# Performance work log

Measured on AMD Instinct MI355X. Metric: run time of the kernel, lower is better.

Reference implementation:

```python
import jax, jax.numpy as jnp
from jax import lax
import numpy as np

B, T, I, H, O = 256, 1024, 64, 25, 64

def setup_inputs() -> dict:
    key = jax.random.key(0)
    ks = jax.random.split(key, 7)
    s_ih = 1.0 / np.sqrt(H)  # PyTorch LSTM init scale (uniform +-1/sqrt(H))
    return {
        "x": jax.random.normal(ks[0], (B, T, I), dtype=jnp.float32),
        "W_ih": jax.random.uniform(ks[1], (4 * H, I), minval=-s_ih, maxval=s_ih, dtype=jnp.float32),
        "W_hh": jax.random.uniform(ks[2], (4 * H, H), minval=-s_ih, maxval=s_ih, dtype=jnp.float32),
        "b_ih": jax.random.uniform(ks[3], (4 * H,), minval=-s_ih, maxval=s_ih, dtype=jnp.float32),
        "b_hh": jax.random.uniform(ks[4], (4 * H,), minval=-s_ih, maxval=s_ih, dtype=jnp.float32),
        "W_fc": jax.random.uniform(ks[5], (O, H), minval=-s_ih, maxval=s_ih, dtype=jnp.float32),
        "b_fc": jax.random.uniform(ks[6], (O,), minval=-s_ih, maxval=s_ih, dtype=jnp.float32),
    }

def reference(x, W_ih, W_hh, b_ih, b_hh, W_fc, b_fc):
    # x: [B, T, I]; PyTorch LSTM gate order: i, f, g, o
    Bh = x.shape[0]
    Hh = W_hh.shape[1]
    # Precompute the input contribution to all gates for all timesteps (one big GEMM).
    gates_x = jnp.einsum('bti,gi->btg', x, W_ih) + b_ih + b_hh  # [B, T, 4H]

    def step(carry, gx):
        h, c = carry
        g = gx + h @ W_hh.T                     # [B, 4H]
        i, f, gg, o = jnp.split(g, 4, axis=-1)
        i = jax.nn.sigmoid(i)
        f = jax.nn.sigmoid(f)
        gg = jnp.tanh(gg)
        o = jax.nn.sigmoid(o)
        c = f * c + i * gg
        h = o * jnp.tanh(c)
        return (h, c), h

    h0 = jnp.zeros((Bh, Hh), dtype=x.dtype)
    c0 = jnp.zeros((Bh, Hh), dtype=x.dtype)
    _, hs = lax.scan(step, (h0, c0), jnp.swapaxes(gates_x, 0, 1))  # hs: [T, B, H]
    hs = jnp.swapaxes(hs, 0, 1)                                   # [B, T, H]
    return hs @ W_fc.T + b_fc                                     # [B, T, O]
```

## Files before the change

kernel.cpp:

```cpp
#include <hip/hip_runtime.h>
#include <hip/hip_fp16.h>


#define Bn 256
#define Tn 1024
#define In 64
#define Hn 25
#define Gn 100
#define On 64
#define BT (Bn * Tn)
#define ROW 100

#define SCL_S -1.44269504089f
#define SCL_T -2.88539008178f

typedef __attribute__((ext_vector_type(8))) short short8;
typedef __attribute__((ext_vector_type(4))) float f32x4;

__device__ __forceinline__ float frcp(float x) { return __builtin_amdgcn_rcpf(x); }
__device__ __forceinline__ float ex2(float x) {
    float r;
    asm("v_exp_f32 %0, %1\n\ts_nop 1" : "=v"(r) : "v"(x));
    return r;
}
__device__ __forceinline__ float bcast(float v, int lane) {
    return __int_as_float(__builtin_amdgcn_readlane(__float_as_int(v), lane));
}
__device__ __forceinline__ float xswap(float x) {
    float a = x, b = x;
    asm("s_nop 0\n\tv_permlane32_swap_b32 %0, %1\n\ts_nop 0"
        : "+v"(a), "+v"(b));
    return b;
}
__device__ __forceinline__ short f2bf(float f) {
    unsigned u = __float_as_uint(f);
    unsigned r = (u + 0x7FFFu + ((u >> 16) & 1u)) >> 16;
    return (short)r;
}

__device__ __forceinline__ void colmap(int n, int& g, float& scl) {
    if (n < 50) {
        const int r = n >> 1;
        g = ((n & 1) ? 2 : 0) * Hn + r;
        scl = (n & 1) ? SCL_T : SCL_S;
    } else {
        const int m = n - 50, r = m >> 1;
        g = ((m & 1) ? 3 : 1) * Hn + r;
        scl = SCL_S;
    }
}

__global__ __launch_bounds__(256)
void prep_w(const float* __restrict__ W_ih, const float* __restrict__ b_ih,
            const float* __restrict__ b_hh, short* __restrict__ wprep,
            float* __restrict__ bprep) {
    const int tid = threadIdx.x;
    for (int i = tid; i < 112 * 64; i += 256) {
        const int n = i >> 6, k = i & 63;
        float v = 0.f;
        if (n < Gn) {
            int g; float scl;
            colmap(n, g, scl);
            v = W_ih[(size_t)g * In + k] * scl;
        }
        wprep[i] = f2bf(v);
    }
    if (tid < 112) {
        float v = 0.f;
        if (tid < Gn) {
            int g; float scl;
            colmap(tid, g, scl);
            v = (b_ih[g] + b_hh[g]) * scl;
        }
        bprep[tid] = v;
    }
}

template <typename ST, bool PREP>
__global__ __launch_bounds__(256, 4)
void gates_mfma(const float* __restrict__ x, const float* __restrict__ W_ih,
                const float* __restrict__ b_ih, const float* __restrict__ b_hh,
                const short* __restrict__ wprep, const float* __restrict__ bprep,
                ST* __restrict__ gws) {
    __shared__ short lA[64 * 72];
    __shared__ short lB[112 * 72];
    __shared__ float lbias[112];

    const int tid = threadIdx.x;
    const size_t row0 = (size_t)blockIdx.x * 64;

    for (int i = tid; i < 64 * 64; i += 256) {
        const int r = i >> 6, k = i & 63;
        lA[r * 72 + k] = f2bf(x[(row0 + r) * In + k]);
    }
    if (PREP) {
        for (int i = tid; i < 112 * 32; i += 256) {
            const int j = 2 * i, n = j >> 6, k = j & 63;
            *(int*)&lB[n * 72 + k] = ((const int*)wprep)[i];
        }
        if (tid < 112) lbias[tid] = bprep[tid];
    } else {
        for (int i = tid; i < 112 * 64; i += 256) {
            const int n = i >> 6, k = i & 63;
            float v = 0.f;
            if (n < Gn) {
                int g; float scl;
                colmap(n, g, scl);
                v = W_ih[(size_t)g * In + k] * scl;
            }
            lB[n * 72 + k] = f2bf(v);
        }
        if (tid < 112) {
            float v = 0.f;
            if (tid < Gn) {
                int g; float scl;
                colmap(tid, g, scl);
                v = (b_ih[g] + b_hh[g]) * scl;
            }
            lbias[tid] = v;
        }
    }
    __syncthreads();

    const int wave = tid >> 6;
    const int lane = tid & 63;
    const int quad = lane >> 4;
    const int l16  = lane & 15;
    const int arow = wave * 16 + l16;

    const short8 a0 = *(const short8*)&lA[arow * 72 + 0  + quad * 8];
    const short8 a1 = *(const short8*)&lA[arow * 72 + 32 + quad * 8];

#pragma unroll
    for (int nt = 0; nt < 7; ++nt) {
        const int col = nt * 16 + l16;
        const short8 b0 = *(const short8*)&lB[col * 72 + 0  + quad * 8];
        const short8 b1 = *(const short8*)&lB[col * 72 + 32 + quad * 8];
        const float bias = lbias[col];
        f32x4 acc = {bias, bias, bias, bias};
        acc = __builtin_amdgcn_mfma_f32_16x16x32_bf16(a0, b0, acc, 0, 0, 0);
        acc = __builtin_amdgcn_mfma_f32_16x16x32_bf16(a1, b1, acc, 0, 0, 0);
        if (col < Gn) {
#pragma unroll
            for (int i = 0; i < 4; ++i) {
                const size_t grow = row0 + wave * 16 + quad * 4 + i;
                gws[grow * ROW + col] = (ST)acc[i];
            }
        }
    }
}

template <typename ST> struct GLD;
template <> struct GLD<float> {
    static __device__ __forceinline__ float2 ld(const float* base, int u) {
        return ((const float2*)base)[u];
    }
};
template <> struct GLD<__half> {
    static __device__ __forceinline__ float2 ld(const __half* base, int u) {
        const __half2 h = ((const __half2*)base)[u];
        return make_float2(__low2float(h), __high2float(h));
    }
};

template <typename ST>
__global__ __launch_bounds__(128, 1)
void lstm_rec10(const ST* __restrict__ gws, const float* __restrict__ W_hh,
                const float* __restrict__ W_fc, const float* __restrict__ b_fc,
                float* __restrict__ out) {
    __shared__ float gbuf[2][800];
    __shared__ float hbuf[16][64];

    const int tid  = threadIdx.x;
    const int wid  = tid >> 6;
    const int lane = tid & 63;
    const int b    = blockIdx.x;

    float wAv[25], wBv[25];
    float c = 0.f, h = 0.f;
    float sB = 1.f, dB = 0.f;
    int coff = 0;
    float wFC[25];
    float bfc = 0.f;
    float* op = nullptr;
    const ST* src = gws + (size_t)b * Tn * ROW;

    if (wid == 0) {
        const bool lo = lane < 32;
        const int rr  = min(lane & 31, Hn - 1);
        const float sclA = SCL_S;
        const float sclB = lo ? SCL_T : SCL_S;
        sB = lo ? 2.f : 1.f;
        dB = lo ? -1.f : 0.f;
        const float* rowA = W_hh + (size_t)((lo ? 0 : 1) * Hn + rr) * Hn;
        const float* rowB = W_hh + (size_t)((lo ? 2 : 3) * Hn + rr) * Hn;
#pragma unroll
        for (int j = 0; j < 25; ++j) {
            wAv[j] = rowA[j] * sclA;
            wBv[j] = rowB[j] * sclB;
        }
        coff = 2 * rr + (lo ? 0 : 50);
    } else {
#pragma unroll
        for (int j = 0; j < 25; ++j) wFC[j] = W_fc[(size_t)lane * Hn + j];
        bfc = b_fc[lane];
        op = out + (size_t)b * Tn * On + lane;

        float2 t0[6]; float2 t6;
#pragma unroll
        for (int i = 0; i < 6; ++i) t0[i] = GLD<ST>::ld(src, lane + 64 * i);
        if (lane < 16) t6 = GLD<ST>::ld(src, 384 + lane);
#pragma unroll
        for (int i = 0; i < 6; ++i)
            *(float2*)&gbuf[0][2 * (lane + 64 * i)] = t0[i];
        if (lane < 16) *(float2*)&gbuf[0][2 * (384 + lane)] = t6;
    }
    asm volatile("s_waitcnt lgkmcnt(0)" ::: "memory");
    __builtin_amdgcn_s_barrier();
    asm volatile("" ::: "memory");

#pragma unroll 1
    for (int k = 0; k < 129; ++k) {
        if (wid == 0) {
            if (k < 128) {
                const int kb = k & 1;
                float2 g[8];
#pragma unroll
                for (int s = 0; s < 8; ++s)
                    g[s] = *(const float2*)&gbuf[kb][s * 100 + coff];
#pragma unroll
                for (int s = 0; s < 8; ++s) {
                    const int t = k * 8 + s;
                    float aA0 = g[s].x, aB0 = g[s].y;
                    float aA1 = 0.f,   aB1 = 0.f;
#pragma unroll
                    for (int j = 0; j < 24; j += 2) {
                        const float h0 = bcast(h, j);
                        const float h1 = bcast(h, j + 1);
                        aA0 = fmaf(wAv[j],     h0, aA0);
                        aB0 = fmaf(wBv[j],     h0, aB0);
                        aA1 = fmaf(wAv[j + 1], h1, aA1);
                        aB1 = fmaf(wBv[j + 1], h1, aB1);
                    }
                    {
                        const float h0 = bcast(h, 24);
                        aA0 = fmaf(wAv[24], h0, aA0);
                        aB0 = fmaf(wBv[24], h0, aB0);
                    }
                    const float aA = aA0 + aA1;
                    const float aB = aB0 + aB1;

                    const float actA = frcp(1.f + ex2(aA));
                    const float actB = sB * frcp(1.f + ex2(aB)) + dB;
                    const float Fg = xswap(actA);
                    const float Og = xswap(actB);
                    c = Fg * c + actA * actB;
                    const float th = 2.f * frcp(1.f + ex2(c * SCL_T)) - 1.f;
                    h = Og * th;

                    hbuf[t & 15][lane] = h;
                }
            }
        } else {
            float2 t0[6]; float2 t6;
            if (k < 127) {
                const ST* s1 = src + (size_t)(k + 1) * 800;
#pragma unroll
                for (int i = 0; i < 6; ++i) t0[i] = GLD<ST>::ld(s1, lane + 64 * i);
                if (lane < 16) t6 = GLD<ST>::ld(s1, 384 + lane);
            }
            if (k >= 1) {
#pragma unroll
                for (int s = 0; s < 8; ++s) {
                    const int t = (k - 1) * 8 + s;
                    const int sl = t & 15;
                    float a0 = bfc, a1 = 0.f;
#pragma unroll
                    for (int j = 0; j < 24; j += 2) {
                        a0 = fmaf(hbuf[sl][j],     wFC[j],     a0);
                        a1 = fmaf(hbuf[sl][j + 1], wFC[j + 1], a1);
                    }
                    a0 = fmaf(hbuf[sl][24], wFC[24], a0);
                    op[(size_t)t * On] = a0 + a1;
                }
            }
            if (k < 127) {
                const int nb = (k + 1) & 1;
#pragma unroll
                for (int i = 0; i < 6; ++i)
                    *(float2*)&gbuf[nb][2 * (lane + 64 * i)] = t0[i];
                if (lane < 16) *(float2*)&gbuf[nb][2 * (384 + lane)] = t6;
            }
        }
        asm volatile("s_waitcnt lgkmcnt(0)" ::: "memory");
        __builtin_amdgcn_s_barrier();
        asm volatile("" ::: "memory");
    }
}

extern "C" void kernel_launch(void* const* d_in, const int* in_sizes, int n_in,
                              void* d_out, int out_size, void* d_ws, size_t ws_size,
                              hipStream_t stream) {
    const float* x    = (const float*)d_in[0];
    const float* W_ih = (const float*)d_in[1];
    const float* W_hh = (const float*)d_in[2];
    const float* b_ih = (const float*)d_in[3];
    const float* b_hh = (const float*)d_in[4];
    const float* W_fc = (const float*)d_in[5];
    const float* b_fc = (const float*)d_in[6];
    float* out = (float*)d_out;

    const size_t need_f32 = (size_t)BT * ROW * sizeof(float);
    const size_t need_h   = (size_t)BT * ROW * sizeof(__half);
    const size_t PREPB    = 16384;
    const int nb1 = BT / 64;

    if (ws_size >= need_f32) {
        float* gws = (float*)d_ws;
        if (ws_size >= need_f32 + PREPB) {
            short* wprep = (short*)((char*)d_ws + need_f32);
            float* bprep = (float*)(wprep + 112 * 64);
            prep_w<<<1, 256, 0, stream>>>(W_ih, b_ih, b_hh, wprep, bprep);
            gates_mfma<float, true><<<nb1, 256, 0, stream>>>(
                x, W_ih, b_ih, b_hh, wprep, bprep, gws);
        } else {
            gates_mfma<float, false><<<nb1, 256, 0, stream>>>(
                x, W_ih, b_ih, b_hh, nullptr, nullptr, gws);
        }
        lstm_rec10<float><<<Bn, 128, 0, stream>>>(gws, W_hh, W_fc, b_fc, out);
    } else {
        __half* gws = (__half*)d_ws;
        if (ws_size >= need_h + PREPB) {
            short* wprep = (short*)((char*)d_ws + need_h);
            float* bprep = (float*)(wprep + 112 * 64);
            prep_w<<<1, 256, 0, stream>>>(W_ih, b_ih, b_hh, wprep, bprep);
            gates_mfma<__half, true><<<nb1, 256, 0, stream>>>(
                x, W_ih, b_ih, b_hh, wprep, bprep, gws);
        } else {
            gates_mfma<__half, false><<<nb1, 256, 0, stream>>>(
                x, W_ih, b_ih, b_hh, nullptr, nullptr, gws);
        }
        lstm_rec10<__half><<<Bn, 128, 0, stream>>>(gws, W_hh, W_fc, b_fc, out);
    }
}
```

Measured before the change: 360.1 us.

## Fuse input-gate GEMM into recurrent LSTM kernel with a third producer wave

Removes the separate gates_mfma and prep_w kernels and the global gate workspace. A third wave per block now computes the x·W_ih gate contributions for the next 8 timesteps with bf16 MFMA, writing straight into the LDS double buffer while the recurrence wave works. This avoids writing and re-reading the large gate buffer through HBM and saves kernel launches. In exchange, each block redoes the weight setup, has a longer per-iteration producer path that could become critical, and occupies 192 threads per block.

```diff
diff --git a/kernel.cpp b/kernel.cpp
--- a/kernel.cpp
+++ b/kernel.cpp
@@ -8,14 +8,13 @@
 #define Hn 25
 #define Gn 100
 #define On 64
-#define BT (Bn * Tn)
-#define ROW 100
 
 #define SCL_S -1.44269504089f
 #define SCL_T -2.88539008178f
 
 typedef __attribute__((ext_vector_type(8))) short short8;
 typedef __attribute__((ext_vector_type(4))) float f32x4;
+typedef __attribute__((ext_vector_type(4))) int i32x4;
 
 __device__ __forceinline__ float frcp(float x) { return __builtin_amdgcn_rcpf(x); }
 __device__ __forceinline__ float ex2(float x) {
@@ -32,10 +31,9 @@
         : "+v"(a), "+v"(b));
     return b;
 }
-__device__ __forceinline__ short f2bf(float f) {
+__device__ __forceinline__ unsigned short f2bf(float f) {
     unsigned u = __float_as_uint(f);
-    unsigned r = (u + 0x7FFFu + ((u >> 16) & 1u)) >> 16;
-    return (short)r;
+    return (unsigned short)((u + 0x7FFFu + ((u >> 16) & 1u)) >> 16);
 }
 
 __device__ __forceinline__ void colmap(int n, int& g, float& scl) {
@@ -50,12 +48,23 @@
     }
 }
 
-__global__ __launch_bounds__(256)
-void prep_w(const float* __restrict__ W_ih, const float* __restrict__ b_ih,
-            const float* __restrict__ b_hh, short* __restrict__ wprep,
-            float* __restrict__ bprep) {
-    const int tid = threadIdx.x;
-    for (int i = tid; i < 112 * 64; i += 256) {
+__global__ __launch_bounds__(192, 1)
+void lstm_fused(const float* __restrict__ x, const float* __restrict__ W_ih,
+                const float* __restrict__ W_hh, const float* __restrict__ b_ih,
+                const float* __restrict__ b_hh, const float* __restrict__ W_fc,
+                const float* __restrict__ b_fc, float* __restrict__ out) {
+    __shared__ short lB[112 * 72];
+    __shared__ float lbias[112];
+    __shared__ short xlds[16 * 72];
+    __shared__ float gbuf[2][800];
+    __shared__ float hbuf[16][64];
+
+    const int tid  = threadIdx.x;
+    const int wid  = tid >> 6;
+    const int lane = tid & 63;
+    const int b    = blockIdx.x;
+
+    for (int i = tid; i < 112 * 64; i += 192) {
         const int n = i >> 6, k = i & 63;
         float v = 0.f;
         if (n < Gn) {
@@ -63,7 +72,7 @@
             colmap(n, g, scl);
             v = W_ih[(size_t)g * In + k] * scl;
         }
-        wprep[i] = f2bf(v);
+        lB[n * 72 + k] = (short)f2bf(v);
     }
     if (tid < 112) {
         float v = 0.f;
@@ -72,109 +81,10 @@
             colmap(tid, g, scl);
             v = (b_ih[g] + b_hh[g]) * scl;
         }
-        bprep[tid] = v;
-    }
-}
-
-template <typename ST, bool PREP>
-__global__ __launch_bounds__(256, 4)
-void gates_mfma(const float* __restrict__ x, const float* __restrict__ W_ih,
-                const float* __restrict__ b_ih, const float* __restrict__ b_hh,
-                const short* __restrict__ wprep, const float* __restrict__ bprep,
-                ST* __restrict__ gws) {
-    __shared__ short lA[64 * 72];
-    __shared__ short lB[112 * 72];
-    __shared__ float lbias[112];
-
-    const int tid = threadIdx.x;
-    const size_t row0 = (size_t)blockIdx.x * 64;
-
-    for (int i = tid; i < 64 * 64; i += 256) {
-        const int r = i >> 6, k = i & 63;
-        lA[r * 72 + k] = f2bf(x[(row0 + r) * In + k]);
-    }
-    if (PREP) {
-        for (int i = tid; i < 112 * 32; i += 256) {
-            const int j = 2 * i, n = j >> 6, k = j & 63;
-            *(int*)&lB[n * 72 + k] = ((const int*)wprep)[i];
-        }
-        if (tid < 112) lbias[tid] = bprep[tid];
-    } else {
-        for (int i = tid; i < 112 * 64; i += 256) {
-            const int n = i >> 6, k = i & 63;
-            float v = 0.f;
-            if (n < Gn) {
-                int g; float scl;
-                colmap(n, g, scl);
-                v = W_ih[(size_t)g * In + k] * scl;
-            }
-            lB[n * 72 + k] = f2bf(v);
-        }
-        if (tid < 112) {
-            float v = 0.f;
-            if (tid < Gn) {
-                int g; float scl;
-                colmap(tid, g, scl);
-                v = (b_ih[g] + b_hh[g]) * scl;
-            }
-            lbias[tid] = v;
-        }
-    }
+        lbias[tid] = v;
+    }
+    for (int i = tid; i < 16 * 72; i += 192) xlds[i] = 0;
     __syncthreads();
-
-    const int wave = tid >> 6;
-    const int lane = tid & 63;
-    const int quad = lane >> 4;
-    const int l16  = lane & 15;
-    const int arow = wave * 16 + l16;
-
-    const short8 a0 = *(const short8*)&lA[arow * 72 + 0  + quad * 8];
-    const short8 a1 = *(const short8*)&lA[arow * 72 + 32 + quad * 8];
-
-#pragma unroll
-    for (int nt = 0; nt < 7; ++nt) {
-        const int col = nt * 16 + l16;
-        const short8 b0 = *(const short8*)&lB[col * 72 + 0  + quad * 8];
-        const short8 b1 = *(const short8*)&lB[col * 72 + 32 + quad * 8];
-        const float bias = lbias[col];
-        f32x4 acc = {bias, bias, bias, bias};
-        acc = __builtin_amdgcn_mfma_f32_16x16x32_bf16(a0, b0, acc, 0, 0, 0);
-        acc = __builtin_amdgcn_mfma_f32_16x16x32_bf16(a1, b1, acc, 0, 0, 0);
-        if (col < Gn) {
-#pragma unroll
-            for (int i = 0; i < 4; ++i) {
-                const size_t grow = row0 + wave * 16 + quad * 4 + i;
-                gws[grow * ROW + col] = (ST)acc[i];
-            }
-        }
-    }
-}
-
-template <typename ST> struct GLD;
-template <> struct GLD<float> {
-    static __device__ __forceinline__ float2 ld(const float* base, int u) {
-        return ((const float2*)base)[u];
-    }
-};
-template <> struct GLD<__half> {
-    static __device__ __forceinline__ float2 ld(const __half* base, int u) {
-        const __half2 h = ((const __half2*)base)[u];
-        return make_float2(__low2float(h), __high2float(h));
-    }
-};
-
-template <typename ST>
-__global__ __launch_bounds__(128, 1)
-void lstm_rec10(const ST* __restrict__ gws, const float* __restrict__ W_hh,
-                const float* __restrict__ W_fc, const float* __restrict__ b_fc,
-                float* __restrict__ out) {
-    __shared__ float gbuf[2][800];
-    __shared__ float hbuf[16][64];
-
-    const int tid  = threadIdx.x;
-    const int wid  = tid >> 6;
-    const int lane = tid & 63;
-    const int b    = blockIdx.x;
 
     float wAv[25], wBv[25];
     float c = 0.f, h = 0.f;
@@ -183,7 +93,13 @@
     float wFC[25];
     float bfc = 0.f;
     float* op = nullptr;
-    const ST* src = gws + (size_t)b * Tn * ROW;
+    short8 bf0[7], bf1[7];
+    float biasv[7];
+    float4 xra, xrb;
+    const float* xb = x + (size_t)b * Tn * In;
+
+    const int quad = lane >> 4;
+    const int l16  = lane & 15;
 
     if (wid == 0) {
         const bool lo = lane < 32;
@@ -200,24 +116,51 @@
             wBv[j] = rowB[j] * sclB;
         }
         coff = 2 * rr + (lo ? 0 : 50);
-    } else {
+    } else if (wid == 1) {
 #pragma unroll
         for (int j = 0; j < 25; ++j) wFC[j] = W_fc[(size_t)lane * Hn + j];
         bfc = b_fc[lane];
         op = out + (size_t)b * Tn * On + lane;
-
-        float2 t0[6]; float2 t6;
-#pragma unroll
-        for (int i = 0; i < 6; ++i) t0[i] = GLD<ST>::ld(src, lane + 64 * i);
-        if (lane < 16) t6 = GLD<ST>::ld(src, 384 + lane);
-#pragma unroll
-        for (int i = 0; i < 6; ++i)
-            *(float2*)&gbuf[0][2 * (lane + 64 * i)] = t0[i];
-        if (lane < 16) *(float2*)&gbuf[0][2 * (384 + lane)] = t6;
-    }
-    asm volatile("s_waitcnt lgkmcnt(0)" ::: "memory");
-    __builtin_amdgcn_s_barrier();
-    asm volatile("" ::: "memory");
+    } else {
+#pragma unroll
+        for (int nt = 0; nt < 7; ++nt) {
+            const int col = nt * 16 + l16;
+            bf0[nt] = *(const short8*)&lB[col * 72 + 0  + quad * 8];
+            bf1[nt] = *(const short8*)&lB[col * 72 + 32 + quad * 8];
+            biasv[nt] = lbias[col];
+        }
+        {
+            const float4 a = *(const float4*)(xb + lane * 8);
+            const float4 d = *(const float4*)(xb + lane * 8 + 4);
+            i32x4 p;
+            p.x = (int)(((unsigned)f2bf(a.y) << 16) | f2bf(a.x));
+            p.y = (int)(((unsigned)f2bf(a.w) << 16) | f2bf(a.z));
+            p.z = (int)(((unsigned)f2bf(d.y) << 16) | f2bf(d.x));
+            p.w = (int)(((unsigned)f2bf(d.w) << 16) | f2bf(d.z));
+            *(i32x4*)&xlds[(lane >> 3) * 72 + (lane & 7) * 8] = p;
+        }
+    }
+    __syncthreads();
+
+    if (wid == 2) {
+        const short8 a0 = *(const short8*)&xlds[l16 * 72 + 0  + quad * 8];
+        const short8 a1 = *(const short8*)&xlds[l16 * 72 + 32 + quad * 8];
+#pragma unroll
+        for (int nt = 0; nt < 7; ++nt) {
+            f32x4 acc = {biasv[nt], biasv[nt], biasv[nt], biasv[nt]};
+            acc = __builtin_amdgcn_mfma_f32_16x16x32_bf16(a0, bf0[nt], acc, 0, 0, 0);
+            acc = __builtin_amdgcn_mfma_f32_16x16x32_bf16(a1, bf1[nt], acc, 0, 0, 0);
+            const int col = nt * 16 + l16;
+            if (lane < 32 && col < Gn) {
+#pragma unroll
+                for (int i = 0; i < 4; ++i)
+                    gbuf[0][(quad * 4 + i) * 100 + col] = acc[i];
+            }
+        }
+        xra = *(const float4*)(xb + 512 + lane * 8);
+        xrb = *(const float4*)(xb + 512 + lane * 8 + 4);
+    }
+    __syncthreads();
 
 #pragma unroll 1
     for (int k = 0; k < 129; ++k) {
@@ -261,14 +204,7 @@
                     hbuf[t & 15][lane] = h;
                 }
             }
-        } else {
-            float2 t0[6]; float2 t6;
-            if (k < 127) {
-                const ST* s1 = src + (size_t)(k + 1) * 800;
-#pragma unroll
-                for (int i = 0; i < 6; ++i) t0[i] = GLD<ST>::ld(s1, lane + 64 * i);
-                if (lane < 16) t6 = GLD<ST>::ld(s1, 384 + lane);
-            }
+        } else if (wid == 1) {
             if (k >= 1) {
 #pragma unroll
                 for (int s = 0; s < 8; ++s) {
@@ -284,12 +220,35 @@
                     op[(size_t)t * On] = a0 + a1;
                 }
             }
+        } else {
             if (k < 127) {
+                i32x4 p;
+                p.x = (int)(((unsigned)f2bf(xra.y) << 16) | f2bf(xra.x));
+                p.y = (int)(((unsigned)f2bf(xra.w) << 16) | f2bf(xra.z));
+                p.z = (int)(((unsigned)f2bf(xrb.y) << 16) | f2bf(xrb.x));
+                p.w = (int)(((unsigned)f2bf(xrb.w) << 16) | f2bf(xrb.z));
+                *(i32x4*)&xlds[(lane >> 3) * 72 + (lane & 7) * 8] = p;
+                if (k < 126) {
+                    const float* xs = xb + (size_t)(k + 2) * 512;
+                    xra = *(const float4*)(xs + lane * 8);
+                    xrb = *(const float4*)(xs + lane * 8 + 4);
+                }
+                asm volatile("s_waitcnt lgkmcnt(0)" ::: "memory");
+                const short8 a0 = *(const short8*)&xlds[l16 * 72 + 0  + quad * 8];
+                const short8 a1 = *(const short8*)&xlds[l16 * 72 + 32 + quad * 8];
                 const int nb = (k + 1) & 1;
 #pragma unroll
-                for (int i = 0; i < 6; ++i)
-                    *(float2*)&gbuf[nb][2 * (lane + 64 * i)] = t0[i];
-                if (lane < 16) *(float2*)&gbuf[nb][2 * (384 + lane)] = t6;
+                for (int nt = 0; nt < 7; ++nt) {
+                    f32x4 acc = {biasv[nt], biasv[nt], biasv[nt], biasv[nt]};
+                    acc = __builtin_amdgcn_mfma_f32_16x16x32_bf16(a0, bf0[nt], acc, 0, 0, 0);
+                    acc = __builtin_amdgcn_mfma_f32_16x16x32_bf16(a1, bf1[nt], acc, 0, 0, 0);
+                    const int col = nt * 16 + l16;
+                    if (lane < 32 && col < Gn) {
+#pragma unroll
+                        for (int i = 0; i < 4; ++i)
+                            gbuf[nb][(quad * 4 + i) * 100 + col] = acc[i];
+                    }
+                }
             }
         }
         asm volatile("s_waitcnt lgkmcnt(0)" ::: "memory");
@@ -310,36 +269,6 @@
     const float* b_fc = (const float*)d_in[6];
     float* out = (float*)d_out;
 
-    const size_t need_f32 = (size_t)BT * ROW * sizeof(float);
-    const size_t need_h   = (size_t)BT * ROW * sizeof(__half);
-    const size_t PREPB    = 16384;
-    const int nb1 = BT / 64;
-
-    if (ws_size >= need_f32) {
-        float* gws = (float*)d_ws;
-        if (ws_size >= need_f32 + PREPB) {
-            short* wprep = (short*)((char*)d_ws + need_f32);
-            float* bprep = (float*)(wprep + 112 * 64);
-            prep_w<<<1, 256, 0, stream>>>(W_ih, b_ih, b_hh, wprep, bprep);
-            gates_mfma<float, true><<<nb1, 256, 0, stream>>>(
-                x, W_ih, b_ih, b_hh, wprep, bprep, gws);
-        } else {
-            gates_mfma<float, false><<<nb1, 256, 0, stream>>>(
-                x, W_ih, b_ih, b_hh, nullptr, nullptr, gws);
-        }
-        lstm_rec10<float><<<Bn, 128, 0, stream>>>(gws, W_hh, W_fc, b_fc, out);
-    } else {
-        __half* gws = (__half*)d_ws;
-        if (ws_size >= need_h + PREPB) {
-            short* wprep = (short*)((char*)d_ws + need_h);
-            float* bprep = (float*)(wprep + 112 * 64);
-            prep_w<<<1, 256, 0, stream>>>(W_ih, b_ih, b_hh, wprep, bprep);
-            gates_mfma<__half, true><<<nb1, 256, 0, stream>>>(
-                x, W_ih, b_ih, b_hh, wprep, bprep, gws);
-        } else {
-            gates_mfma<__half, false><<<nb1, 256, 0, stream>>>(
-                x, W_ih, b_ih, b_hh, nullptr, nullptr, gws);
-        }
-        lstm_rec10<__half><<<Bn, 128, 0, stream>>>(gws, W_hh, W_fc, b_fc, out);
-    }
-}
+    lstm_fused<<<Bn, 192, 0, stream>>>(x, W_ih, W_hh, b_ih, b_hh,
+                                       W_fc, b_fc, out);
+}
```

After: 310.5 us. 13.8% less time.
